# Kernel tuning notes

Hardware: AMD Instinct MI355X
Metric: run time of the kernel (lower is better)

Reference implementation:

```python
import jax, jax.numpy as jnp
import numpy as np
from jax import lax

B, C, H, W = 2, 64, 64, 64


def _conv1x1(x, w, b):
    # w: [Cout, Cin], x: [B, Cin, H, W]
    return jnp.einsum('oi,bihw->bohw', w, x) + b[None, :, None, None]


def _conv3x3(x, w, b):
    # w: [Cout, Cin, 3, 3]
    y = lax.conv_general_dilated(x, w, (1, 1), 'SAME',
                                 dimension_numbers=('NCHW', 'OIHW', 'NCHW'))
    return y + b[None, :, None, None]


def _bn(x, s, b, m, v, eps=1e-5):
    # eval-mode batchnorm with running stats
    inv = s / jnp.sqrt(v + eps)
    return x * inv[None, :, None, None] + (b - m * inv)[None, :, None, None]


def _prelu(x, a):
    return jnp.where(x > 0, x, a * x)


def _forward(x, g,
             pam_q_w, pam_q_b, pam_k_w, pam_k_b, pam_v_w, pam_v_b,
             pam_qg_w, pam_qg_b, pam_kg_w, pam_kg_b, gamma_p,
             se_fc1_w, se_fc2_w, gamma_c,
             pconv1_w, pconv1_b, pbn1_s, pbn1_b, pbn1_m, pbn1_v, pprelu1,
             pconv2_w, pconv2_b, pbn2_s, pbn2_b, pbn2_m, pbn2_v, pprelu2,
             cconv1_w, cconv1_b, cbn1_s, cbn1_b, cbn1_m, cbn1_v, cprelu1,
             cconv2_w, cconv2_b, cbn2_s, cbn2_b, cbn2_m, cbn2_v, cprelu2,
             fconv_w, fconv_b, fbn_s, fbn_b, fbn_m, fbn_v, fprelu):
    b, c, h, w = x.shape
    n = h * w
    sm = jax.nn.softmax
    # ---- G_PAM: position attention with guided double softmax ----
    q = _conv1x1(x, pam_q_w, pam_q_b).reshape(b, c, n)
    k = _conv1x1(x, pam_k_w, pam_k_b).reshape(b, c, n)
    v = _conv1x1(x, pam_v_w, pam_v_b).reshape(b, c, n)
    qg = _conv1x1(g, pam_qg_w, pam_qg_b).reshape(b, -1, n)
    kg = _conv1x1(g, pam_kg_w, pam_kg_b).reshape(b, -1, n)
    att = sm(jnp.einsum('bcn,bcm->bnm', q, k), axis=-1)        # [B,N,N]
    att_g = sm(jnp.einsum('bcn,bcm->bnm', qg, kg), axis=-1)    # [B,N,N]
    gatt = sm(jnp.einsum('bnk,bkm->bnm', att, att_g), axis=-1) # [B,N,N]
    pam_o = jnp.einsum('bcm,bnm->bcn', v, gatt).reshape(b, c, h, w)
    pam = gamma_p * pam_o + x
    # ---- pconv head ----
    t = _prelu(_bn(_conv3x3(pam, pconv1_w, pconv1_b), pbn1_s, pbn1_b, pbn1_m, pbn1_v), pprelu1)
    pam2 = _prelu(_bn(_conv1x1(t, pconv2_w, pconv2_b), pbn2_s, pbn2_b, pbn2_m, pbn2_v), pprelu2)
    # ---- G_CAM: channel attention with SE-gated guide ----
    xq = pam2.reshape(b, c, n)
    att_c = sm(jnp.einsum('bcn,bdn->bcd', xq, xq), axis=-1)    # [B,C,C]
    gy = g.mean((2, 3))  # SE: [B,C]
    gy = jax.nn.sigmoid(jnp.einsum('oc,bc->bo', se_fc2_w,
                                   jax.nn.relu(jnp.einsum('rc,bc->br', se_fc1_w, gy))))
    gq = (g * gy[:, :, None, None]).reshape(b, c, n)
    att_cg = sm(jnp.einsum('bcn,bdn->bcd', gq, gq), axis=-1)   # [B,C,C]
    ge = jnp.einsum('bck,bkd->bcd', att_c, att_cg)
    ge = jnp.max(ge, axis=-1, keepdims=True) - ge
    gatt_c = sm(ge, axis=-1)
    cam_o = jnp.einsum('bcd,bdn->bcn', gatt_c, xq).reshape(b, c, h, w)
    cam = gamma_c * cam_o + pam2
    # ---- cconv + fconv heads ----
    t = _prelu(_bn(_conv3x3(cam, cconv1_w, cconv1_b), cbn1_s, cbn1_b, cbn1_m, cbn1_v), cprelu1)
    cam2 = _prelu(_bn(_conv1x1(t, cconv2_w, cconv2_b), cbn2_s, cbn2_b, cbn2_m, cbn2_v), cprelu2)
    final = _prelu(_bn(_conv1x1(cam2, fconv_w, fconv_b), fbn_s, fbn_b, fbn_m, fbn_v), fprelu)
    return final


def setup_inputs() -> dict:
    key = jax.random.key(0)
    keys = iter(jax.random.split(key, 64))
    nk = lambda: next(keys)
    f32 = jnp.float32
    nrm = lambda shape, s=0.1: s * jax.random.normal(nk(), shape, f32)
    d = {}
    d['x'] = jax.random.normal(nk(), (B, C, H, W), f32)
    d['g'] = jax.random.normal(nk(), (B, C, H, W), f32)
    for p in ['pam_q', 'pam_k', 'pam_v', 'pam_qg', 'pam_kg']:
        d[p + '_w'] = nrm((C, C))
        d[p + '_b'] = nrm((C,))
    d['gamma_p'] = jnp.asarray(0.5, f32)
    d['se_fc1_w'] = nrm((C // 2, C))
    d['se_fc2_w'] = nrm((C, C // 2))
    d['gamma_c'] = jnp.asarray(0.5, f32)
    for pre in ['p', 'c']:
        d[pre + 'conv1_w'] = nrm((C, C, 3, 3), 0.05)
        d[pre + 'conv1_b'] = nrm((C,))
        d[pre + 'bn1_s'] = 1.0 + nrm((C,))
        d[pre + 'bn1_b'] = nrm((C,))
        d[pre + 'bn1_m'] = nrm((C,))
        d[pre + 'bn1_v'] = 1.0 + 0.1 * jax.random.uniform(nk(), (C,), f32)
        d[pre + 'prelu1'] = jnp.asarray(0.25, f32)
        d[pre + 'conv2_w'] = nrm((C, C))
        d[pre + 'conv2_b'] = nrm((C,))
        d[pre + 'bn2_s'] = 1.0 + nrm((C,))
        d[pre + 'bn2_b'] = nrm((C,))
        d[pre + 'bn2_m'] = nrm((C,))
        d[pre + 'bn2_v'] = 1.0 + 0.1 * jax.random.uniform(nk(), (C,), f32)
        d[pre + 'prelu2'] = jnp.asarray(0.25, f32)
    d['fconv_w'] = nrm((C, C))
    d['fconv_b'] = nrm((C,))
    d['fbn_s'] = 1.0 + nrm((C,))
    d['fbn_b'] = nrm((C,))
    d['fbn_m'] = nrm((C,))
    d['fbn_v'] = 1.0 + 0.1 * jax.random.uniform(nk(), (C,), f32)
    d['fprelu'] = jnp.asarray(0.25, f32)
    return d


def reference(x, g,
              pam_q_w, pam_q_b, pam_k_w, pam_k_b, pam_v_w, pam_v_b,
              pam_qg_w, pam_qg_b, pam_kg_w, pam_kg_b, gamma_p,
              se_fc1_w, se_fc2_w, gamma_c,
              pconv1_w, pconv1_b, pbn1_s, pbn1_b, pbn1_m, pbn1_v, pprelu1,
              pconv2_w, pconv2_b, pbn2_s, pbn2_b, pbn2_m, pbn2_v, pprelu2,
              cconv1_w, cconv1_b, cbn1_s, cbn1_b, cbn1_m, cbn1_v, cprelu1,
              cconv2_w, cconv2_b, cbn2_s, cbn2_b, cbn2_m, cbn2_v, cprelu2,
              fconv_w, fconv_b, fbn_s, fbn_b, fbn_m, fbn_v, fprelu):
    return _forward(x, g,
                    pam_q_w, pam_q_b, pam_k_w, pam_k_b, pam_v_w, pam_v_b,
                    pam_qg_w, pam_qg_b, pam_kg_w, pam_kg_b, gamma_p,
                    se_fc1_w, se_fc2_w, gamma_c,
                    pconv1_w, pconv1_b, pbn1_s, pbn1_b, pbn1_m, pbn1_v, pprelu1,
                    pconv2_w, pconv2_b, pbn2_s, pbn2_b, pbn2_m, pbn2_v, pprelu2,
                    cconv1_w, cconv1_b, cbn1_s, cbn1_b, cbn1_m, cbn1_v, cprelu1,
                    cconv2_w, cconv2_b, cbn2_s, cbn2_b, cbn2_m, cbn2_v, cprelu2,
                    fconv_w, fconv_b, fbn_s, fbn_b, fbn_m, fbn_v, fprelu)
```

## Files before the change

### kernel.cpp

```cpp
#include <hip/hip_runtime.h>
#include <hip/hip_fp8.h>


typedef float f32x4 __attribute__((ext_vector_type(4)));
typedef __bf16 bf16x8 __attribute__((ext_vector_type(8)));
typedef int int4v __attribute__((ext_vector_type(4)));
typedef int int8v __attribute__((ext_vector_type(8)));
typedef unsigned short ushort8 __attribute__((ext_vector_type(8)));
typedef unsigned char uchar8 __attribute__((ext_vector_type(8)));

#define DI __device__ __forceinline__

DI float bf2f(unsigned short u) { union { unsigned int i; float f; } x; x.i = ((unsigned int)u) << 16; return x.f; }
DI unsigned short f2bf(float f) { union { float f; unsigned int i; } x; x.f = f; unsigned int r = x.i + 0x7fff + ((x.i >> 16) & 1); return (unsigned short)(r >> 16); }
DI unsigned char f2fp8(float f) { __hip_fp8_e4m3 h(f); return (unsigned char)h.__x; }
DI float sane(float x) { return (x > -1e8f) ? ((x < 1e8f) ? x : 1e8f) : -1e8f; }

DI void async16(const unsigned short* g, unsigned short* l) {
    __builtin_amdgcn_global_load_lds(
        (const __attribute__((address_space(1))) void*)g,
        (__attribute__((address_space(3))) void*)l, 16, 0, 0);
}
DI void async16b(const unsigned char* g, unsigned char* l) {
    __builtin_amdgcn_global_load_lds(
        (const __attribute__((address_space(1))) void*)g,
        (__attribute__((address_space(3))) void*)l, 16, 0, 0);
}

__global__ __launch_bounds__(256) void diag_fill(float* __restrict__ out, int n, float val)
{
    int i = blockIdx.x * 256 + threadIdx.x;
    if (i < n) out[i] = val;
}

__global__ __launch_bounds__(256) void gemm_score(
    const unsigned short* __restrict__ A,
    const unsigned short* __restrict__ B,
    unsigned short* __restrict__ C, int N, long abStride, long cStride)
{
    A += (long)blockIdx.z * abStride;
    B += (long)blockIdx.z * abStride;
    C += (long)blockIdx.z * cStride;
    const int tid  = threadIdx.x;
    const int bm   = blockIdx.y, bn = blockIdx.x;
    const int lane = tid & 63, wid = tid >> 6;
    const int wm   = (wid >> 1) * 64, wn = (wid & 1) * 64;
    const int l16  = lane & 15, quad = lane >> 4;

    f32x4 acc[4][4] = {};
    bf16x8 af[2][4], bfr[2][4];
    #pragma unroll
    for (int w = 0; w < 2; w++) {
        #pragma unroll
        for (int i = 0; i < 4; i++)
            af[w][i]  = *(const bf16x8*)&A[(long)(bm * 128 + wm + i * 16 + l16) * 64 + w * 32 + quad * 8];
        #pragma unroll
        for (int j = 0; j < 4; j++)
            bfr[w][j] = *(const bf16x8*)&B[(long)(bn * 128 + wn + j * 16 + l16) * 64 + w * 32 + quad * 8];
    }
    #pragma unroll
    for (int w = 0; w < 2; w++)
        #pragma unroll
        for (int i = 0; i < 4; i++)
            #pragma unroll
            for (int j = 0; j < 4; j++)
                acc[i][j] = __builtin_amdgcn_mfma_f32_16x16x32_bf16(af[w][i], bfr[w][j], acc[i][j], 0, 0, 0);

    #pragma unroll
    for (int i = 0; i < 4; i++) {
        int rb = bm * 128 + wm + i * 16 + quad * 4;
        #pragma unroll
        for (int j = 0; j < 4; j++) {
            int col = bn * 128 + wn + j * 16 + l16;
            #pragma unroll
            for (int r = 0; r < 4; r++)
                C[(long)(rb + r) * N + col] = f2bf(acc[i][j][r]);
        }
    }
}

__global__ __launch_bounds__(256, 3) void gemm_nt(
    const unsigned short* __restrict__ A,
    const unsigned short* __restrict__ B,
    float* __restrict__ C,
    int M, int N, int K, long sA, long sB, long sC)
{
    A += (long)blockIdx.z * sA;
    B += (long)blockIdx.z * sB;
    C += (long)blockIdx.z * sC;
    __shared__ __align__(16) unsigned short As[128 * 32];
    __shared__ __align__(16) unsigned short Bs[128 * 32];
    const int tid  = threadIdx.x;
    const int bn   = blockIdx.x, slice = blockIdx.y;
    const int lane = tid & 63, wid = tid >> 6;
    const int wm   = (wid >> 1) * 64, wn = (wid & 1) * 64;
    const int l16  = lane & 15, quad = lane >> 4;

    f32x4 acc[4][4] = {};

    const int Kc   = K / (int)gridDim.y;
    const int kbeg = slice * Kc;
    const int nIter = Kc / 32;

    const int row0 = tid >> 2,        cp0 = tid & 3;
    const int row1 = (tid + 256) >> 2, cp1 = (tid + 256) & 3;
    int ar0 = row0; if (ar0 > M - 1) ar0 = M - 1;
    int ar1 = row1; if (ar1 > M - 1) ar1 = M - 1;
    const unsigned short* pa0 = &A[(long)ar0 * K + kbeg + ((cp0 ^ (row0 & 3)) * 8)];
    const unsigned short* pa1 = &A[(long)ar1 * K + kbeg + ((cp1 ^ (row1 & 3)) * 8)];
    const unsigned short* pb0 = &B[(long)(bn * 128 + row0) * K + kbeg + ((cp0 ^ (row0 & 3)) * 8)];
    const unsigned short* pb1 = &B[(long)(bn * 128 + row1) * K + kbeg + ((cp1 ^ (row1 & 3)) * 8)];
    unsigned short* la0 = &As[row0 * 32 + cp0 * 8];
    unsigned short* la1 = &As[row1 * 32 + cp1 * 8];
    unsigned short* lb0 = &Bs[row0 * 32 + cp0 * 8];
    unsigned short* lb1 = &Bs[row1 * 32 + cp1 * 8];

    const int sw = (quad ^ (l16 & 3)) * 8;

    for (int it = 0; it < nIter; it++) {
        __syncthreads();
        async16(pa0, la0);
        async16(pa1, la1);
        async16(pb0, lb0);
        async16(pb1, lb1);
        pa0 += 32; pa1 += 32; pb0 += 32; pb1 += 32;
        __syncthreads();
        bf16x8 af[4], bfr[4];
        #pragma unroll
        for (int i = 0; i < 4; i++) af[i]  = *(const bf16x8*)&As[(wm + i * 16 + l16) * 32 + sw];
        #pragma unroll
        for (int j = 0; j < 4; j++) bfr[j] = *(const bf16x8*)&Bs[(wn + j * 16 + l16) * 32 + sw];
        #pragma unroll
        for (int i = 0; i < 4; i++)
            #pragma unroll
            for (int j = 0; j < 4; j++)
                acc[i][j] = __builtin_amdgcn_mfma_f32_16x16x32_bf16(af[i], bfr[j], acc[i][j], 0, 0, 0);
    }

    #pragma unroll
    for (int i = 0; i < 4; i++) {
        int rb = wm + i * 16 + quad * 4;
        #pragma unroll
        for (int j = 0; j < 4; j++) {
            int col = bn * 128 + wn + j * 16 + l16;
            #pragma unroll
            for (int r = 0; r < 4; r++) {
                int row = rb + r;
                if (row < M)
                    C[(long)slice * M * N + (long)row * N + col] = acc[i][j][r];
            }
        }
    }
}

__global__ __launch_bounds__(256, 2) void gemm_p8(
    const unsigned char* __restrict__ A,
    const unsigned char* __restrict__ B,
    unsigned short* __restrict__ C, int N, int K,
    long sA, long sB, long sC)
{
    A += (long)blockIdx.z * sA;
    B += (long)blockIdx.z * sB;
    C += (long)blockIdx.z * sC;
    __shared__ __align__(16) unsigned char As[128 * 256];
    __shared__ __align__(16) unsigned char Bs[128 * 256];
    const int tid  = threadIdx.x;
    const int bm   = blockIdx.y, bn = blockIdx.x;
    const int lane = tid & 63, wid = tid >> 6;
    const int wm   = (wid >> 1) * 64, wn = (wid & 1) * 64;
    const int l16  = lane & 15, quad = lane >> 4;

    f32x4 acc[4][4] = {};

    const int srow = tid >> 4;
    const int sp   = tid & 15;
    const int cp   = sp ^ (srow & 15);
    const unsigned char* pa = &A[(long)(bm * 128 + srow) * K + cp * 16];
    const unsigned char* pb = &B[(long)(bn * 128 + srow) * K + cp * 16];
    unsigned char* la = &As[srow * 256 + sp * 16];
    unsigned char* lb = &Bs[srow * 256 + sp * 16];
    const long gstep = 16L * K;

    const int nIter = K / 256;
    for (int it = 0; it < nIter; it++) {
        __syncthreads();
        #pragma unroll
        for (int m = 0; m < 8; m++) {
            async16b(pa + m * gstep, la + m * 4096);
            async16b(pb + m * gstep, lb + m * 4096);
        }
        pa += 256; pb += 256;
        __syncthreads();
        #pragma unroll
        for (int h = 0; h < 2; h++) {
            const int c0 = h * 8 + 2 * quad;
            const int s0 = (c0 ^ (l16 & 15)) * 16;
            const int s1 = ((c0 + 1) ^ (l16 & 15)) * 16;
            int8v bfr[4];
            #pragma unroll
            for (int j = 0; j < 4; j++) {
                const unsigned char* base = &Bs[(wn + j * 16 + l16) * 256];
                int4v v0 = *(const int4v*)(base + s0);
                int4v v1 = *(const int4v*)(base + s1);
                bfr[j][0] = v0[0]; bfr[j][1] = v0[1]; bfr[j][2] = v0[2]; bfr[j][3] = v0[3];
                bfr[j][4] = v1[0]; bfr[j][5] = v1[1]; bfr[j][6] = v1[2]; bfr[j][7] = v1[3];
            }
            #pragma unroll
            for (int i = 0; i < 4; i++) {
                const unsigned char* base = &As[(wm + i * 16 + l16) * 256];
                int4v v0 = *(const int4v*)(base + s0);
                int4v v1 = *(const int4v*)(base + s1);
                int8v af;
                af[0] = v0[0]; af[1] = v0[1]; af[2] = v0[2]; af[3] = v0[3];
                af[4] = v1[0]; af[5] = v1[1]; af[6] = v1[2]; af[7] = v1[3];
                #pragma unroll
                for (int j = 0; j < 4; j++)
                    acc[i][j] = __builtin_amdgcn_mfma_scale_f32_16x16x128_f8f6f4(
                        af, bfr[j], acc[i][j],
                        0, 0, 0, 0x7f7f7f7f, 0, 0x7f7f7f7f);
            }
        }
    }

    const float ds = 1.f / 65536.f;
    #pragma unroll
    for (int i = 0; i < 4; i++) {
        int rb = bm * 128 + wm + i * 16 + quad * 4;
        #pragma unroll
        for (int j = 0; j < 4; j++) {
            int col = bn * 128 + wn + j * 16 + l16;
            #pragma unroll
            for (int r = 0; r < 4; r++)
                C[(long)(rb + r) * N + col] = f2bf(acc[i][j][r] * ds);
        }
    }
}

__global__ __launch_bounds__(256) void row_softmax(unsigned short* __restrict__ buf, long bStride)
{
    unsigned short* p = buf + (long)blockIdx.y * bStride + (long)blockIdx.x * 4096;
    const int tid = threadIdx.x, lane = tid & 63, wid = tid >> 6;
    float v[16]; float mx = -1e30f;
    #pragma unroll
    for (int t = 0; t < 16; t++) {
        float x = sane(bf2f(p[t * 256 + tid]));
        v[t] = x; mx = fmaxf(mx, x);
    }
    #pragma unroll
    for (int o = 32; o; o >>= 1) mx = fmaxf(mx, __shfl_xor(mx, o, 64));
    __shared__ float rmax[4], rsum[4];
    if (!lane) rmax[wid] = mx;
    __syncthreads();
    mx = fmaxf(fmaxf(rmax[0], rmax[1]), fmaxf(rmax[2], rmax[3]));
    float s = 0.f;
    #pragma unroll
    for (int t = 0; t < 16; t++) { v[t] = __expf(v[t] - mx); s += v[t]; }
    #pragma unroll
    for (int o = 32; o; o >>= 1) s += __shfl_xor(s, o, 64);
    if (!lane) rsum[wid] = s;
    __syncthreads();
    s = rsum[0] + rsum[1] + rsum[2] + rsum[3];
    float inv = 1.f / s;
    #pragma unroll
    for (int t = 0; t < 16; t++) p[t * 256 + tid] = f2bf(v[t] * inv);
}

__global__ __launch_bounds__(256) void row_softmax_f8(
    const unsigned short* __restrict__ in, unsigned char* __restrict__ out,
    long inStride, long outStride)
{
    const unsigned short* p = in + (long)blockIdx.y * inStride + (long)blockIdx.x * 4096;
    unsigned char* q = out + (long)blockIdx.y * outStride + (long)blockIdx.x * 4096;
    const int tid = threadIdx.x, lane = tid & 63, wid = tid >> 6;
    float v[16]; float mx = -1e30f;
    #pragma unroll
    for (int t = 0; t < 16; t++) {
        float x = sane(bf2f(p[t * 256 + tid]));
        v[t] = x; mx = fmaxf(mx, x);
    }
    #pragma unroll
    for (int o = 32; o; o >>= 1) mx = fmaxf(mx, __shfl_xor(mx, o, 64));
    __shared__ float rmax[4], rsum[4];
    if (!lane) rmax[wid] = mx;
    __syncthreads();
    mx = fmaxf(fmaxf(rmax[0], rmax[1]), fmaxf(rmax[2], rmax[3]));
    float s = 0.f;
    #pragma unroll
    for (int t = 0; t < 16; t++) { v[t] = __expf(v[t] - mx); s += v[t]; }
    #pragma unroll
    for (int o = 32; o; o >>= 1) s += __shfl_xor(s, o, 64);
    if (!lane) rsum[wid] = s;
    __syncthreads();
    s = rsum[0] + rsum[1] + rsum[2] + rsum[3];
    float inv = 256.f / s;
    #pragma unroll
    for (int t = 0; t < 16; t++) q[t * 256 + tid] = f2fp8(v[t] * inv);
}

__global__ __launch_bounds__(256) void colsm_partial(
    const unsigned short* __restrict__ buf,
    float* __restrict__ pmx, float* __restrict__ psum,
    long bufStride, long pStride)
{
    buf  += (long)blockIdx.z * bufStride;
    pmx  += (long)blockIdx.z * pStride;
    psum += (long)blockIdx.z * pStride;
    const int tid = threadIdx.x;
    const int colgrp = tid & 63, rg = tid >> 6;
    const int cbase = blockIdx.x * 512 + colgrp * 8;
    const int r0 = blockIdx.y * 128 + rg * 32;
    const unsigned short* p = buf + (long)r0 * 4096 + cbase;
    float mx[8], s[8];
    #pragma unroll
    for (int j = 0; j < 8; j++) { mx[j] = -1e30f; s[j] = 0.f; }
    for (int r = 0; r < 32; r++) {
        ushort8 v = *(const ushort8*)(p + (long)r * 4096);
        #pragma unroll
        for (int j = 0; j < 8; j++) {
            float x = sane(bf2f(v[j]));
            float nm = fmaxf(mx[j], x);
            s[j] = s[j] * __expf(mx[j] - nm) + __expf(x - nm);
            mx[j] = nm;
        }
    }
    __shared__ float smx[4][512], ssm[4][512];
    #pragma unroll
    for (int j = 0; j < 8; j++) { smx[rg][colgrp * 8 + j] = mx[j]; ssm[rg][colgrp * 8 + j] = s[j]; }
    __syncthreads();
    for (int c = tid; c < 512; c += 256) {
        float M = fmaxf(fmaxf(smx[0][c], smx[1][c]), fmaxf(smx[2][c], smx[3][c]));
        float S = 0.f;
        #pragma unroll
        for (int i = 0; i < 4; i++) S += ssm[i][c] * __expf(smx[i][c] - M);
        int col = blockIdx.x * 512 + c;
        pmx[blockIdx.y * 4096 + col] = M;
        psum[blockIdx.y * 4096 + col] = S;
    }
}

__global__ __launch_bounds__(256) void colsm_norm_f8(
    const unsigned short* __restrict__ in, unsigned char* __restrict__ out,
    const float* __restrict__ pmx, const float* __restrict__ psum,
    long inStride, long outStride, long pStride)
{
    in   += (long)blockIdx.z * inStride;
    out  += (long)blockIdx.z * outStride;
    pmx  += (long)blockIdx.z * pStride;
    psum += (long)blockIdx.z * pStride;
    const int tid = threadIdx.x;
    const int colgrp = tid & 63, rg = tid >> 6;
    const int cbase = blockIdx.x * 512 + colgrp * 8;
    const int r0 = blockIdx.y * 128 + rg * 32;
    const unsigned short* p = in + (long)r0 * 4096 + cbase;
    unsigned char* q = out + (long)r0 * 4096 + cbase;
    float M[8], inv[8];
    #pragma unroll
    for (int j = 0; j < 8; j++) M[j] = -1e30f;
    for (int ch = 0; ch < 32; ch++) {
        #pragma unroll
        for (int j = 0; j < 8; j++) M[j] = fmaxf(M[j], pmx[ch * 4096 + cbase + j]);
    }
    float S[8];
    #pragma unroll
    for (int j = 0; j < 8; j++) S[j] = 0.f;
    for (int ch = 0; ch < 32; ch++) {
        #pragma unroll
        for (int j = 0; j < 8; j++)
            S[j] += psum[ch * 4096 + cbase + j] * __expf(pmx[ch * 4096 + cbase + j] - M[j]);
    }
    #pragma unroll
    for (int j = 0; j < 8; j++) inv[j] = 256.f / S[j];
    for (int r = 0; r < 32; r++) {
        ushort8 v = *(const ushort8*)(p + (long)r * 4096);
        uchar8 o;
        #pragma unroll
        for (int j = 0; j < 8; j++) o[j] = f2fp8(__expf(sane(bf2f(v[j])) - M[j]) * inv[j]);
        *(uchar8*)(q + (long)r * 4096) = o;
    }
}

__global__ __launch_bounds__(256) void proj_x3(
    const float* __restrict__ X,
    const float* __restrict__ Wq, const float* __restrict__ bq,
    const float* __restrict__ Wk, const float* __restrict__ bk,
    const float* __restrict__ Wv, const float* __restrict__ bv,
    unsigned short* __restrict__ qT, unsigned short* __restrict__ kT,
    unsigned short* __restrict__ vC)
{
    const int b = blockIdx.y, nt = blockIdx.x, tid = threadIdx.x;
    __shared__ float Xs[64][64];
    __shared__ float Wqs[64][65];
    __shared__ float Wks[64][65];
    __shared__ float Wvs[64][64];
    __shared__ float Bq[64], Bk[64], Bv[64];
    for (int f = tid; f < 4096; f += 256) {
        int i = f >> 6, n = f & 63;
        Xs[i][n] = X[((long)b * 64 + i) * 4096 + nt * 64 + n];
        Wqs[f & 63][f >> 6] = Wq[f];
        Wks[f & 63][f >> 6] = Wk[f];
        Wvs[f >> 6][f & 63] = Wv[f];
    }
    if (tid < 64) { Bq[tid] = bq[tid]; Bk[tid] = bk[tid]; Bv[tid] = bv[tid]; }
    __syncthreads();
    const int c = tid & 63, g = tid >> 6;
    {
        float acc[16];
        #pragma unroll
        for (int j = 0; j < 16; j++) acc[j] = Bq[c];
        for (int i = 0; i < 64; i++) {
            float wv = Wqs[i][c];
            #pragma unroll
            for (int j = 0; j < 16; j++) acc[j] += wv * Xs[i][g + 4 * j];
        }
        unsigned short* ob = qT + ((long)b * 4096 + nt * 64) * 64;
        #pragma unroll
        for (int j = 0; j < 16; j++) ob[(g + 4 * j) * 64 + c] = f2bf(acc[j]);
    }
    {
        float acc[16];
        #pragma unroll
        for (int j = 0; j < 16; j++) acc[j] = Bk[c];
        for (int i = 0; i < 64; i++) {
            float wv = Wks[i][c];
            #pragma unroll
            for (int j = 0; j < 16; j++) acc[j] += wv * Xs[i][g + 4 * j];
        }
        unsigned short* ob = kT + ((long)b * 4096 + nt * 64) * 64;
        #pragma unroll
        for (int j = 0; j < 16; j++) ob[(g + 4 * j) * 64 + c] = f2bf(acc[j]);
    }
    {
        const int n = tid & 63, gg = tid >> 6;
        float acc[16];
        #pragma unroll
        for (int j = 0; j < 16; j++) acc[j] = Bv[gg + 4 * j];
        for (int i = 0; i < 64; i++) {
            float xv = Xs[i][n];
            #pragma unroll
            for (int j = 0; j < 16; j++) acc[j] += Wvs[gg + 4 * j][i] * xv;
        }
        unsigned short* ob = vC + ((long)b * 64) * 4096 + nt * 64;
        #pragma unroll
        for (int j = 0; j < 16; j++) ob[(long)(gg + 4 * j) * 4096 + n] = f2bf(acc[j]);
    }
}

__global__ __launch_bounds__(256) void proj_g2(
    const float* __restrict__ G,
    const float* __restrict__ Wq, const float* __restrict__ bq,
    const float* __restrict__ Wk, const float* __restrict__ bk,
    unsigned short* __restrict__ qgT, unsigned short* __restrict__ kgT)
{
    const int b = blockIdx.y, nt = blockIdx.x, tid = threadIdx.x;
    __shared__ float Xs[64][64];
    __shared__ float Wqs[64][65];
    __shared__ float Wks[64][65];
    __shared__ float Bq[64], Bk[64];
    for (int f = tid; f < 4096; f += 256) {
        int i = f >> 6, n = f & 63;
        Xs[i][n] = G[((long)b * 64 + i) * 4096 + nt * 64 + n];
        Wqs[f & 63][f >> 6] = Wq[f];
        Wks[f & 63][f >> 6] = Wk[f];
    }
    if (tid < 64) { Bq[tid] = bq[tid]; Bk[tid] = bk[tid]; }
    __syncthreads();
    const int c = tid & 63, g = tid >> 6;
    {
        float acc[16];
        #pragma unroll
        for (int j = 0; j < 16; j++) acc[j] = Bq[c];
        for (int i = 0; i < 64; i++) {
            float wv = Wqs[i][c];
            #pragma unroll
            for (int j = 0; j < 16; j++) acc[j] += wv * Xs[i][g + 4 * j];
        }
        unsigned short* ob = qgT + ((long)b * 4096 + nt * 64) * 64;
        #pragma unroll
        for (int j = 0; j < 16; j++) ob[(g + 4 * j) * 64 + c] = f2bf(acc[j]);
    }
    {
        float acc[16];
        #pragma unroll
        for (int j = 0; j < 16; j++) acc[j] = Bk[c];
        for (int i = 0; i < 64; i++) {
            float wv = Wks[i][c];
            #pragma unroll
            for (int j = 0; j < 16; j++) acc[j] += wv * Xs[i][g + 4 * j];
        }
        unsigned short* ob = kgT + ((long)b * 4096 + nt * 64) * 64;
        #pragma unroll
        for (int j = 0; j < 16; j++) ob[(g + 4 * j) * 64 + c] = f2bf(acc[j]);
    }
}

__global__ __launch_bounds__(256) void combine_pam(
    const float* __restrict__ part, const float* __restrict__ x,
    const float* __restrict__ gammaPtr, float* __restrict__ pam, int nsplit,
    long sPart, long sX)
{
    part += (long)blockIdx.y * sPart;
    x    += (long)blockIdx.y * sX;
    pam  += (long)blockIdx.y * sX;
    int i = blockIdx.x * 256 + threadIdx.x;
    float s = 0.f;
    for (int k = 0; k < nsplit; k++) s += part[(long)k * 262144 + i];
    pam[i] = gammaPtr[0] * s + x[i];
}

__global__ __launch_bounds__(256) void conv3x3_bn(
    const float* __restrict__ X, const float* __restrict__ W9,
    const float* __restrict__ bias,
    const float* __restrict__ bns, const float* __restrict__ bnb,
    const float* __restrict__ bnm, const float* __restrict__ bnv,
    const float* __restrict__ prelu, float* __restrict__ out)
{
    const int b = blockIdx.y, h = blockIdx.x, co0 = blockIdx.z * 16, tid = threadIdx.x;
    __shared__ float Ls[3][64][66];
    __shared__ float ep0[64], ep1[64], ep2[64];
    __shared__ float alpha;
    for (int f = tid; f < 3 * 64 * 64; f += 256) {
        int ky = f >> 12, rem = f & 4095, ci = rem >> 6, w = rem & 63;
        int hh = h + ky - 1;
        Ls[ky][ci][w + 1] = (hh >= 0 && hh < 64) ? X[(((long)b * 64 + ci) * 64 + hh) * 64 + w] : 0.f;
    }
    for (int f = tid; f < 192; f += 256) {
        int ky = f >> 6, ci = f & 63;
        Ls[ky][ci][0] = 0.f; Ls[ky][ci][65] = 0.f;
    }
    if (tid < 64) {
        float inv = bns[tid] * rsqrtf(fmaxf(bnv[tid], 0.f) + 1e-5f);
        ep0[tid] = inv; ep1[tid] = bnb[tid] - bnm[tid] * inv; ep2[tid] = bias[tid];
    }
    if (tid == 0) alpha = prelu[0];
    __syncthreads();
    const int w = tid & 63, g = tid >> 6;
    float acc[4];
    #pragma unroll
    for (int j = 0; j < 4; j++) acc[j] = ep2[co0 + g * 4 + j];
    for (int ci = 0; ci < 64; ci++) {
        float v0 = Ls[0][ci][w], v1 = Ls[0][ci][w + 1], v2 = Ls[0][ci][w + 2];
        float v3 = Ls[1][ci][w], v4 = Ls[1][ci][w + 1], v5 = Ls[1][ci][w + 2];
        float v6 = Ls[2][ci][w], v7 = Ls[2][ci][w + 1], v8 = Ls[2][ci][w + 2];
        #pragma unroll
        for (int j = 0; j < 4; j++) {
            const float* wp = &W9[((co0 + g * 4 + j) * 64 + ci) * 9];
            acc[j] += wp[0] * v0 + wp[1] * v1 + wp[2] * v2
                    + wp[3] * v3 + wp[4] * v4 + wp[5] * v5
                    + wp[6] * v6 + wp[7] * v7 + wp[8] * v8;
        }
    }
    #pragma unroll
    for (int j = 0; j < 4; j++) {
        int co = co0 + g * 4 + j;
        float y = acc[j] * ep0[co] + ep1[co];
        y = y > 0.f ? y : alpha * y;
        out[(((long)b * 64 + co) * 64 + h) * 64 + w] = y;
    }
}

__global__ __launch_bounds__(256) void conv1x1_bn(
    const float* __restrict__ X, const float* __restrict__ W,
    const float* __restrict__ bias,
    const float* __restrict__ bns, const float* __restrict__ bnb,
    const float* __restrict__ bnm, const float* __restrict__ bnv,
    const float* __restrict__ prelu, float* __restrict__ out)
{
    const int b = blockIdx.y, nt = blockIdx.x, co0 = blockIdx.z * 16, tid = threadIdx.x;
    __shared__ float Xs[64][64];
    __shared__ float Ws[16][64];
    __shared__ float ep0[16], ep1[16], ep2[16];
    __shared__ float alpha;
    for (int f = tid; f < 4096; f += 256) {
        int i = f >> 6, n = f & 63;
        Xs[i][n] = X[((long)b * 64 + i) * 4096 + nt * 64 + n];
    }
    for (int f = tid; f < 1024; f += 256)
        Ws[f >> 6][f & 63] = W[(co0 + (f >> 6)) * 64 + (f & 63)];
    if (tid < 16) {
        int c = co0 + tid;
        float inv = bns[c] * rsqrtf(fmaxf(bnv[c], 0.f) + 1e-5f);
        ep0[tid] = inv; ep1[tid] = bnb[c] - bnm[c] * inv; ep2[tid] = bias[c];
    }
    if (tid == 0) alpha = prelu[0];
    __syncthreads();
    const int n = tid & 63, g = tid >> 6;
    float acc[4];
    #pragma unroll
    for (int j = 0; j < 4; j++) acc[j] = ep2[g * 4 + j];
    for (int i = 0; i < 64; i++) {
        float xv = Xs[i][n];
        #pragma unroll
        for (int j = 0; j < 4; j++) acc[j] += Ws[g * 4 + j][i] * xv;
    }
    #pragma unroll
    for (int j = 0; j < 4; j++) {
        int lc = g * 4 + j;
        float y = acc[j] * ep0[lc] + ep1[lc];
        y = y > 0.f ? y : alpha * y;
        out[((long)b * 64 + co0 + lc) * 4096 + nt * 64 + n] = y;
    }
}

__global__ __launch_bounds__(256) void conv1x1x2(
    const float* __restrict__ X,
    const float* __restrict__ W1, const float* __restrict__ b1,
    const float* __restrict__ s1, const float* __restrict__ bb1,
    const float* __restrict__ m1, const float* __restrict__ v1,
    const float* __restrict__ p1,
    const float* __restrict__ W2, const float* __restrict__ b2,
    const float* __restrict__ s2, const float* __restrict__ bb2,
    const float* __restrict__ m2, const float* __restrict__ v2,
    const float* __restrict__ p2,
    float* __restrict__ out)
{
    const int b = blockIdx.y, nt = blockIdx.x, tid = threadIdx.x;
    __shared__ float Xs[64][33];
    __shared__ float Y1[64][33];
    __shared__ float W1s[64][64], W2s[64][64];
    __shared__ float e0a[64], e1a[64], e2a[64], e0b[64], e1b[64], e2b[64];
    __shared__ float al1, al2;
    for (int f = tid; f < 2048; f += 256) {
        int i = f >> 5, n = f & 31;
        Xs[i][n] = X[((long)b * 64 + i) * 4096 + nt * 32 + n];
    }
    for (int f = tid; f < 4096; f += 256) {
        W1s[f >> 6][f & 63] = W1[f];
        W2s[f >> 6][f & 63] = W2[f];
    }
    if (tid < 64) {
        float inv = s1[tid] * rsqrtf(fmaxf(v1[tid], 0.f) + 1e-5f);
        e0a[tid] = inv; e1a[tid] = bb1[tid] - m1[tid] * inv; e2a[tid] = b1[tid];
        inv = s2[tid] * rsqrtf(fmaxf(v2[tid], 0.f) + 1e-5f);
        e0b[tid] = inv; e1b[tid] = bb2[tid] - m2[tid] * inv; e2b[tid] = b2[tid];
    }
    if (tid == 0) { al1 = p1[0]; al2 = p2[0]; }
    __syncthreads();
    const int n = tid & 31, g = tid >> 5;
    float acc[8];
    #pragma unroll
    for (int j = 0; j < 8; j++) acc[j] = e2a[g * 8 + j];
    for (int i = 0; i < 64; i++) {
        float xv = Xs[i][n];
        #pragma unroll
        for (int j = 0; j < 8; j++) acc[j] += W1s[g * 8 + j][i] * xv;
    }
    #pragma unroll
    for (int j = 0; j < 8; j++) {
        int c = g * 8 + j;
        float y = acc[j] * e0a[c] + e1a[c];
        Y1[c][n] = y > 0.f ? y : al1 * y;
    }
    __syncthreads();
    #pragma unroll
    for (int j = 0; j < 8; j++) acc[j] = e2b[g * 8 + j];
    for (int i = 0; i < 64; i++) {
        float xv = Y1[i][n];
        #pragma unroll
        for (int j = 0; j < 8; j++) acc[j] += W2s[g * 8 + j][i] * xv;
    }
    #pragma unroll
    for (int j = 0; j < 8; j++) {
        int c = g * 8 + j;
        float y = acc[j] * e0b[c] + e1b[c];
        y = y > 0.f ? y : al2 * y;
        out[((long)b * 64 + c) * 4096 + nt * 32 + n] = y;
    }
}

__global__ __launch_bounds__(256) void gram_partial(
    const float* __restrict__ X, float* __restrict__ out, float* __restrict__ gy)
{
    const int ch = blockIdx.x, b = blockIdx.y, tid = threadIdx.x;
    __shared__ float Xs[64][33];
    for (int f = tid; f < 2048; f += 256) {
        int ci = f >> 5, kk = f & 31;
        Xs[ci][kk] = X[((long)b * 64 + ci) * 4096 + ch * 32 + kk];
    }
    __syncthreads();
    const int d = tid & 63, g = tid >> 6;
    float acc[16] = {};
    for (int kk = 0; kk < 32; kk++) {
        float xd = Xs[d][kk];
        #pragma unroll
        for (int j = 0; j < 16; j++) acc[j] += Xs[g + 4 * j][kk] * xd;
    }
    #pragma unroll
    for (int j = 0; j < 16; j++)
        atomicAdd(&out[((long)b * 64 + (g + 4 * j)) * 64 + d], acc[j]);
    if (gy && tid < 64) {
        float s = 0.f;
        for (int kk = 0; kk < 32; kk++) s += Xs[tid][kk];
        atomicAdd(&gy[b * 64 + tid], s);
    }
}

__global__ __launch_bounds__(64) void cam_small(
    const float* __restrict__ gramx, const float* __restrict__ gramg,
    const float* __restrict__ gy_in, const float* __restrict__ fc1,
    const float* __restrict__ fc2, float* __restrict__ gattc)
{
    const int b = blockIdx.x, tid = threadIdx.x;
    __shared__ float Ac[64][65], Acg[64][65];
    __shared__ float gyv[64], r1[32], gys[64];
    gyv[tid] = gy_in[b * 64 + tid] * (1.f / 4096.f);
    __syncthreads();
    if (tid < 32) {
        float s = 0.f;
        for (int c = 0; c < 64; c++) s += fc1[tid * 64 + c] * gyv[c];
        r1[tid] = fmaxf(s, 0.f);
    }
    __syncthreads();
    {
        float s = 0.f;
        for (int r = 0; r < 32; r++) s += fc2[tid * 32 + r] * r1[r];
        gys[tid] = 1.f / (1.f + __expf(-sane(s)));
    }
    __syncthreads();
    {
        const float* r = gramx + ((long)b * 64 + tid) * 64;
        float mx = -1e30f;
        for (int d = 0; d < 64; d++) mx = fmaxf(mx, sane(r[d]));
        float s = 0.f;
        for (int d = 0; d < 64; d++) s += __expf(sane(r[d]) - mx);
        float inv = 1.f / s;
        for (int d = 0; d < 64; d++) Ac[tid][d] = __expf(sane(r[d]) - mx) * inv;
    }
    {
        const float* r = gramg + ((long)b * 64 + tid) * 64;
        float gc = gys[tid];
        float mx = -1e30f;
        for (int d = 0; d < 64; d++) mx = fmaxf(mx, sane(gc * gys[d] * r[d]));
        float s = 0.f;
        for (int d = 0; d < 64; d++) s += __expf(sane(gc * gys[d] * r[d]) - mx);
        float inv = 1.f / s;
        for (int d = 0; d < 64; d++) Acg[tid][d] = __expf(sane(gc * gys[d] * r[d]) - mx) * inv;
    }
    __syncthreads();
    float ge[64];
    float mx1 = -1e30f, mn = 1e30f;
    for (int d = 0; d < 64; d++) {
        float s = 0.f;
        for (int k = 0; k < 64; k++) s += Ac[tid][k] * Acg[k][d];
        ge[d] = s;
        mx1 = fmaxf(mx1, s); mn = fminf(mn, s);
    }
    float M2 = mx1 - mn;
    float s = 0.f;
    for (int d = 0; d < 64; d++) s += __expf((mx1 - ge[d]) - M2);
    float inv = 1.f / s;
    for (int d = 0; d < 64; d++)
        gattc[((long)b * 64 + tid) * 64 + d] = __expf((mx1 - ge[d]) - M2) * inv;
}

__global__ __launch_bounds__(256) void cam_apply(
    const float* __restrict__ pam2, const float* __restrict__ gattc,
    const float* __restrict__ gammaPtr, float* __restrict__ cam)
{
    const int b = blockIdx.y, nt = blockIdx.x, co0 = blockIdx.z * 16, tid = threadIdx.x;
    __shared__ float Xs[64][64];
    __shared__ float Gt[16][64];
    for (int f = tid; f < 4096; f += 256) {
        int d = f >> 6, n = f & 63;
        Xs[d][n] = pam2[((long)b * 64 + d) * 4096 + nt * 64 + n];
    }
    for (int f = tid; f < 1024; f += 256)
        Gt[f >> 6][f & 63] = gattc[((long)b * 64 + co0 + (f >> 6)) * 64 + (f & 63)];
    __syncthreads();
    const float gamma = gammaPtr[0];
    const int n = tid & 63, g = tid >> 6;
    float acc[4] = {};
    for (int d = 0; d < 64; d++) {
        float xv = Xs[d][n];
        #pragma unroll
        for (int j = 0; j < 4; j++) acc[j] += Gt[g * 4 + j][d] * xv;
    }
    #pragma unroll
    for (int j = 0; j < 4; j++) {
        int c = co0 + g * 4 + j;
        cam[((long)b * 64 + c) * 4096 + nt * 64 + n] = gamma * acc[j] + Xs[c][n];
    }
}

extern "C" void kernel_launch(void* const* d_in, const int* in_sizes, int n_in,
                              void* d_out, int out_size, void* d_ws, size_t ws_size,
                              hipStream_t stream)
{
    static const int exp_sizes[51] = {
        524288, 524288,
        4096, 64, 4096, 64, 4096, 64, 4096, 64, 4096, 64,
        1, 2048, 2048, 1,
        36864, 64, 64, 64, 64, 64, 1,
        4096, 64, 64, 64, 64, 64, 1,
        36864, 64, 64, 64, 64, 64, 1,
        4096, 64, 64, 64, 64, 64, 1,
        4096, 64, 64, 64, 64, 64, 1
    };
    bool map_ok = (n_in == 51) && (out_size == 524288);
    if (map_ok) for (int i = 0; i < 51; i++) if (in_sizes[i] != exp_sizes[i]) { map_ok = false; break; }

    const int diag_grid = (out_size + 255) / 256;
    if (!map_ok) {
        diag_fill<<<diag_grid, 256, 0, stream>>>((float*)d_out, out_size, 400.0f);
        return;
    }
    const size_t NEED_FULL = 121000000;
    if (ws_size < NEED_FULL) {
        float code = (ws_size >= 88000000) ? 100.0f : (ws_size >= 55000000 ? 200.0f : 300.0f);
        diag_fill<<<diag_grid, 256, 0, stream>>>((float*)d_out, out_size, code);
        return;
    }
    const bool big = (ws_size >= 248000000);
    const int nb = big ? 2 : 1;
    const long NN = 4096L * 4096;

    auto IN = [&](int i) { return (const float*)d_in[i]; };
    const float* X = IN(0);
    const float* G = IN(1);

    char* wp_ = (char*)d_ws;
    auto alloc = [&](size_t bytes) -> void* {
        void* p = (void*)wp_;
        wp_ += (bytes + 255) & ~(size_t)255;
        return p;
    };
    unsigned short* qT   = (unsigned short*)alloc(2L * 4096 * 64 * 2);
    unsigned short* kT   = (unsigned short*)alloc(2L * 4096 * 64 * 2);
    unsigned short* qgT  = (unsigned short*)alloc(2L * 4096 * 64 * 2);
    unsigned short* kgT  = (unsigned short*)alloc(2L * 4096 * 64 * 2);
    unsigned short* vC   = (unsigned short*)alloc(2L * 64 * 4096 * 2);
    float* part  = (float*)alloc((8L * nb) * 64 * 4096 * 4);
    float* pam   = (float*)alloc(2L * 64 * 4096 * 4);
    float* tbuf  = (float*)alloc(2L * 64 * 4096 * 4);
    float* pam2  = (float*)alloc(2L * 64 * 4096 * 4);
    float* cam   = (float*)alloc(2L * 64 * 4096 * 4);
    float* gramx = (float*)alloc(2L * 64 * 64 * 4);
    float* gramg = (float*)alloc(2L * 64 * 64 * 4);
    float* gy    = (float*)alloc(2L * 64 * 4);
    float* gattc = (float*)alloc(2L * 64 * 64 * 4);
    float* pmx   = (float*)alloc((32L * nb) * 4096 * 4);
    float* psum  = (float*)alloc((32L * nb) * 4096 * 4);
    unsigned short* pbuf   = (unsigned short*)alloc(NN * 2 * nb);
    unsigned short* attS   = (unsigned short*)alloc(NN * 2 * nb);
    unsigned char*  attF8  = (unsigned char*)alloc(NN * nb);
    unsigned char*  attgF8 = (unsigned char*)alloc(NN * nb);

    proj_x3<<<dim3(64, 2), 256, 0, stream>>>(X, IN(2), IN(3), IN(4), IN(5), IN(6), IN(7), qT, kT, vC);
    proj_g2<<<dim3(64, 2), 256, 0, stream>>>(G, IN(8), IN(9), IN(10), IN(11), qgT, kgT);

    const long abStr = 4096L * 64;
    const long pStr  = big ? NN : 0;
    const long pmStr = big ? 32L * 4096 : 0;
    for (int b = 0; b < 2; b += nb) {
        const unsigned short* qTb  = qT  + (long)b * abStr;
        const unsigned short* kTb  = kT  + (long)b * abStr;
        const unsigned short* qgTb = qgT + (long)b * abStr;
        const unsigned short* kgTb = kgT + (long)b * abStr;
        gemm_score<<<dim3(32, 32, nb), 256, 0, stream>>>(qTb,  kTb,  pbuf, 4096, abStr, pStr);
        gemm_score<<<dim3(32, 32, nb), 256, 0, stream>>>(kgTb, qgTb, attS, 4096, abStr, pStr);
        row_softmax_f8<<<dim3(4096, nb), 256, 0, stream>>>(pbuf, attF8, pStr, pStr);
        colsm_partial<<<dim3(8, 32, nb), 256, 0, stream>>>(attS, pmx, psum, pStr, pmStr);
        colsm_norm_f8<<<dim3(8, 32, nb), 256, 0, stream>>>(attS, attgF8, pmx, psum, pStr, pStr, pmStr);
        gemm_p8<<<dim3(32, 32, nb), 256, 0, stream>>>(attF8, attgF8, pbuf, 4096, 4096, pStr, pStr, pStr);
        row_softmax<<<dim3(4096, nb), 256, 0, stream>>>(pbuf, pStr);
        gemm_nt<<<dim3(32, 8, nb), 256, 0, stream>>>(vC + (long)b * abStr, pbuf, part,
                                                     64, 4096, 4096,
                                                     abStr, pStr, big ? 8L * 262144 : 0);
        combine_pam<<<dim3(1024, nb), 256, 0, stream>>>(part, X + (long)b * 262144, IN(12),
                                                        pam + (long)b * 262144, 8,
                                                        big ? 8L * 262144 : 0,
                                                        big ? 262144L : 0);
    }

    conv3x3_bn<<<dim3(64, 2, 4), 256, 0, stream>>>(pam, IN(16), IN(17), IN(18), IN(19), IN(20), IN(21), IN(22), tbuf);
    conv1x1_bn<<<dim3(64, 2, 4), 256, 0, stream>>>(tbuf, IN(23), IN(24), IN(25), IN(26), IN(27), IN(28), IN(29), pam2);

    diag_fill<<<65, 256, 0, stream>>>(gramx, 16384 + 128, 0.0f);
    gram_partial<<<dim3(128, 2), 256, 0, stream>>>(pam2, gramx, nullptr);
    gram_partial<<<dim3(128, 2), 256, 0, stream>>>(G,    gramg, gy);
    cam_small<<<2, 64, 0, stream>>>(gramx, gramg, gy, IN(13), IN(14), gattc);
    cam_apply<<<dim3(64, 2, 4), 256, 0, stream>>>(pam2, gattc, IN(15), cam);

    conv3x3_bn<<<dim3(64, 2, 4), 256, 0, stream>>>(cam, IN(30), IN(31), IN(32), IN(33), IN(34), IN(35), IN(36), pam);
    conv1x1x2<<<dim3(128, 2), 256, 0, stream>>>(pam,
        IN(37), IN(38), IN(39), IN(40), IN(41), IN(42), IN(43),
        IN(44), IN(45), IN(46), IN(47), IN(48), IN(49), IN(50),
        (float*)d_out);
}
```

Before: 657.7 us.

## Compute PAM value GEMM in fp8 with fp8 softmax output and V

Stores the V projection and the final attention softmax in fp8 and replaces the bf16 V×attention GEMM with a new fp8 scaled-MFMA kernel using wider tiles. The combine step applies a descale factor. This halves memory traffic for the attention matrix read and softmax write, but adds fp8 quantization error on V and the attention weights.

```diff
diff --git a/kernel.cpp b/kernel.cpp
--- a/kernel.cpp
+++ b/kernel.cpp
@@ -75,80 +75,6 @@
             #pragma unroll
             for (int r = 0; r < 4; r++)
                 C[(long)(rb + r) * N + col] = f2bf(acc[i][j][r]);
-        }
-    }
-}
-
-__global__ __launch_bounds__(256, 3) void gemm_nt(
-    const unsigned short* __restrict__ A,
-    const unsigned short* __restrict__ B,
-    float* __restrict__ C,
-    int M, int N, int K, long sA, long sB, long sC)
-{
-    A += (long)blockIdx.z * sA;
-    B += (long)blockIdx.z * sB;
-    C += (long)blockIdx.z * sC;
-    __shared__ __align__(16) unsigned short As[128 * 32];
-    __shared__ __align__(16) unsigned short Bs[128 * 32];
-    const int tid  = threadIdx.x;
-    const int bn   = blockIdx.x, slice = blockIdx.y;
-    const int lane = tid & 63, wid = tid >> 6;
-    const int wm   = (wid >> 1) * 64, wn = (wid & 1) * 64;
-    const int l16  = lane & 15, quad = lane >> 4;
-
-    f32x4 acc[4][4] = {};
-
-    const int Kc   = K / (int)gridDim.y;
-    const int kbeg = slice * Kc;
-    const int nIter = Kc / 32;
-
-    const int row0 = tid >> 2,        cp0 = tid & 3;
-    const int row1 = (tid + 256) >> 2, cp1 = (tid + 256) & 3;
-    int ar0 = row0; if (ar0 > M - 1) ar0 = M - 1;
-    int ar1 = row1; if (ar1 > M - 1) ar1 = M - 1;
-    const unsigned short* pa0 = &A[(long)ar0 * K + kbeg + ((cp0 ^ (row0 & 3)) * 8)];
-    const unsigned short* pa1 = &A[(long)ar1 * K + kbeg + ((cp1 ^ (row1 & 3)) * 8)];
-    const unsigned short* pb0 = &B[(long)(bn * 128 + row0) * K + kbeg + ((cp0 ^ (row0 & 3)) * 8)];
-    const unsigned short* pb1 = &B[(long)(bn * 128 + row1) * K + kbeg + ((cp1 ^ (row1 & 3)) * 8)];
-    unsigned short* la0 = &As[row0 * 32 + cp0 * 8];
-    unsigned short* la1 = &As[row1 * 32 + cp1 * 8];
-    unsigned short* lb0 = &Bs[row0 * 32 + cp0 * 8];
-    unsigned short* lb1 = &Bs[row1 * 32 + cp1 * 8];
-
-    const int sw = (quad ^ (l16 & 3)) * 8;
-
-    for (int it = 0; it < nIter; it++) {
-        __syncthreads();
-        async16(pa0, la0);
-        async16(pa1, la1);
-        async16(pb0, lb0);
-        async16(pb1, lb1);
-        pa0 += 32; pa1 += 32; pb0 += 32; pb1 += 32;
-        __syncthreads();
-        bf16x8 af[4], bfr[4];
-        #pragma unroll
-        for (int i = 0; i < 4; i++) af[i]  = *(const bf16x8*)&As[(wm + i * 16 + l16) * 32 + sw];
-        #pragma unroll
-        for (int j = 0; j < 4; j++) bfr[j] = *(const bf16x8*)&Bs[(wn + j * 16 + l16) * 32 + sw];
-        #pragma unroll
-        for (int i = 0; i < 4; i++)
-            #pragma unroll
-            for (int j = 0; j < 4; j++)
-                acc[i][j] = __builtin_amdgcn_mfma_f32_16x16x32_bf16(af[i], bfr[j], acc[i][j], 0, 0, 0);
-    }
-
-    #pragma unroll
-    for (int i = 0; i < 4; i++) {
-        int rb = wm + i * 16 + quad * 4;
-        #pragma unroll
-        for (int j = 0; j < 4; j++) {
-            int col = bn * 128 + wn + j * 16 + l16;
-            #pragma unroll
-            for (int r = 0; r < 4; r++) {
-                int row = rb + r;
-                if (row < M)
-                    C[(long)slice * M * N + (long)row * N + col] = acc[i][j][r];
-            }
         }
     }
 }
@@ -236,33 +162,87 @@
     }
 }
 
-__global__ __launch_bounds__(256) void row_softmax(unsigned short* __restrict__ buf, long bStride)
-{
-    unsigned short* p = buf + (long)blockIdx.y * bStride + (long)blockIdx.x * 4096;
-    const int tid = threadIdx.x, lane = tid & 63, wid = tid >> 6;
-    float v[16]; float mx = -1e30f;
-    #pragma unroll
-    for (int t = 0; t < 16; t++) {
-        float x = sane(bf2f(p[t * 256 + tid]));
-        v[t] = x; mx = fmaxf(mx, x);
-    }
-    #pragma unroll
-    for (int o = 32; o; o >>= 1) mx = fmaxf(mx, __shfl_xor(mx, o, 64));
-    __shared__ float rmax[4], rsum[4];
-    if (!lane) rmax[wid] = mx;
-    __syncthreads();
-    mx = fmaxf(fmaxf(rmax[0], rmax[1]), fmaxf(rmax[2], rmax[3]));
-    float s = 0.f;
-    #pragma unroll
-    for (int t = 0; t < 16; t++) { v[t] = __expf(v[t] - mx); s += v[t]; }
-    #pragma unroll
-    for (int o = 32; o; o >>= 1) s += __shfl_xor(s, o, 64);
-    if (!lane) rsum[wid] = s;
-    __syncthreads();
-    s = rsum[0] + rsum[1] + rsum[2] + rsum[3];
-    float inv = 1.f / s;
-    #pragma unroll
-    for (int t = 0; t < 16; t++) p[t * 256 + tid] = f2bf(v[t] * inv);
+__global__ __launch_bounds__(256, 2) void gemm_p8_pam(
+    const unsigned char* __restrict__ A,
+    const unsigned char* __restrict__ B,
+    float* __restrict__ C,
+    int N, int K, long sA, long sB, long sC)
+{
+    A += (long)blockIdx.z * sA;
+    B += (long)blockIdx.z * sB;
+    C += (long)blockIdx.z * sC;
+    __shared__ __align__(16) unsigned char As[64 * 128];
+    __shared__ __align__(16) unsigned char Bs[256 * 128];
+    const int tid  = threadIdx.x;
+    const int bn   = blockIdx.x, slice = blockIdx.y;
+    const int lane = tid & 63, wid = tid >> 6;
+    const int wn   = wid * 64;
+    const int l16  = lane & 15, quad = lane >> 4;
+
+    f32x4 acc[4][4] = {};
+
+    const int Kc   = K / (int)gridDim.y;
+    const int kbeg = slice * Kc;
+
+    const int arow = tid >> 3, asp = tid & 7, acp = asp ^ (arow & 7);
+    const int brow = tid >> 3, bsp = tid & 7, bcp = bsp ^ (brow & 7);
+    const unsigned char* pa = &A[(long)(arow) * K + kbeg + acp * 16];
+    const unsigned char* pb = &B[(long)(bn * 256 + brow) * K + kbeg + bcp * 16];
+    unsigned char* la = &As[arow * 128 + asp * 16];
+    unsigned char* lb = &Bs[brow * 128 + bsp * 16];
+    const long gstepA = 32L * K;
+    const long gstepB = 32L * K;
+
+    const int s0 = ((2 * quad) ^ (l16 & 7)) * 16;
+    const int s1 = ((2 * quad + 1) ^ (l16 & 7)) * 16;
+
+    const int nIter = Kc / 128;
+    for (int it = 0; it < nIter; it++) {
+        __syncthreads();
+        #pragma unroll
+        for (int m = 0; m < 2; m++)
+            async16b(pa + m * gstepA, la + m * 4096);
+        #pragma unroll
+        for (int m = 0; m < 8; m++)
+            async16b(pb + m * gstepB, lb + m * 4096);
+        pa += 128; pb += 128;
+        __syncthreads();
+        int8v bfr[4];
+        #pragma unroll
+        for (int j = 0; j < 4; j++) {
+            const unsigned char* base = &Bs[(wn + j * 16 + l16) * 128];
+            int4v v0 = *(const int4v*)(base + s0);
+            int4v v1 = *(const int4v*)(base + s1);
+            bfr[j][0] = v0[0]; bfr[j][1] = v0[1]; bfr[j][2] = v0[2]; bfr[j][3] = v0[3];
+            bfr[j][4] = v1[0]; bfr[j][5] = v1[1]; bfr[j][6] = v1[2]; bfr[j][7] = v1[3];
+        }
+        #pragma unroll
+        for (int i = 0; i < 4; i++) {
+            const unsigned char* base = &As[(i * 16 + l16) * 128];
+            int4v v0 = *(const int4v*)(base + s0);
+            int4v v1 = *(const int4v*)(base + s1);
+            int8v af;
+            af[0] = v0[0]; af[1] = v0[1]; af[2] = v0[2]; af[3] = v0[3];
+            af[4] = v1[0]; af[5] = v1[1]; af[6] = v1[2]; af[7] = v1[3];
+            #pragma unroll
+            for (int j = 0; j < 4; j++)
+                acc[i][j] = __builtin_amdgcn_mfma_scale_f32_16x16x128_f8f6f4(
+                    af, bfr[j], acc[i][j],
+                    0, 0, 0, 0x7f7f7f7f, 0, 0x7f7f7f7f);
+        }
+    }
+
+    #pragma unroll
+    for (int i = 0; i < 4; i++) {
+        int rb = i * 16 + quad * 4;
+        #pragma unroll
+        for (int j = 0; j < 4; j++) {
+            int col = bn * 256 + wn + j * 16 + l16;
+            #pragma unroll
+            for (int r = 0; r < 4; r++)
+                C[(long)slice * 64 * N + (long)(rb + r) * N + col] = acc[i][j][r];
+        }
+    }
 }
 
 __global__ __launch_bounds__(256) void row_softmax_f8(
@@ -385,7 +365,7 @@
     const float* __restrict__ Wk, const float* __restrict__ bk,
     const float* __restrict__ Wv, const float* __restrict__ bv,
     unsigned short* __restrict__ qT, unsigned short* __restrict__ kT,
-    unsigned short* __restrict__ vC)
+    unsigned char* __restrict__ vC8)
 {
     const int b = blockIdx.y, nt = blockIdx.x, tid = threadIdx.x;
     __shared__ float Xs[64][64];
@@ -439,9 +419,9 @@
             #pragma unroll
             for (int j = 0; j < 16; j++) acc[j] += Wvs[gg + 4 * j][i] * xv;
         }
-        unsigned short* ob = vC + ((long)b * 64) * 4096 + nt * 64;
-        #pragma unroll
-        for (int j = 0; j < 16; j++) ob[(long)(gg + 4 * j) * 4096 + n] = f2bf(acc[j]);
+        unsigned char* ob = vC8 + ((long)b * 64) * 4096 + nt * 64;
+        #pragma unroll
+        for (int j = 0; j < 16; j++) ob[(long)(gg + 4 * j) * 4096 + n] = f2fp8(acc[j]);
     }
 }
 
@@ -496,7 +476,7 @@
 __global__ __launch_bounds__(256) void combine_pam(
     const float* __restrict__ part, const float* __restrict__ x,
     const float* __restrict__ gammaPtr, float* __restrict__ pam, int nsplit,
-    long sPart, long sX)
+    long sPart, long sX, float ds)
 {
     part += (long)blockIdx.y * sPart;
     x    += (long)blockIdx.y * sX;
@@ -504,7 +484,7 @@
     int i = blockIdx.x * 256 + threadIdx.x;
     float s = 0.f;
     for (int k = 0; k < nsplit; k++) s += part[(long)k * 262144 + i];
-    pam[i] = gammaPtr[0] * s + x[i];
+    pam[i] = gammaPtr[0] * (s * ds) + x[i];
 }
 
 __global__ __launch_bounds__(256) void conv3x3_bn(
@@ -827,7 +807,7 @@
     unsigned short* kT   = (unsigned short*)alloc(2L * 4096 * 64 * 2);
     unsigned short* qgT  = (unsigned short*)alloc(2L * 4096 * 64 * 2);
     unsigned short* kgT  = (unsigned short*)alloc(2L * 4096 * 64 * 2);
-    unsigned short* vC   = (unsigned short*)alloc(2L * 64 * 4096 * 2);
+    unsigned char*  vC8  = (unsigned char*)alloc(2L * 64 * 4096);
     float* part  = (float*)alloc((8L * nb) * 64 * 4096 * 4);
     float* pam   = (float*)alloc(2L * 64 * 4096 * 4);
     float* tbuf  = (float*)alloc(2L * 64 * 4096 * 4);
@@ -844,7 +824,7 @@
     unsigned char*  attF8  = (unsigned char*)alloc(NN * nb);
     unsigned char*  attgF8 = (unsigned char*)alloc(NN * nb);
 
-    proj_x3<<<dim3(64, 2), 256, 0, stream>>>(X, IN(2), IN(3), IN(4), IN(5), IN(6), IN(7), qT, kT, vC);
+    proj_x3<<<dim3(64, 2), 256, 0, stream>>>(X, IN(2), IN(3), IN(4), IN(5), IN(6), IN(7), qT, kT, vC8);
     proj_g2<<<dim3(64, 2), 256, 0, stream>>>(G, IN(8), IN(9), IN(10), IN(11), qgT, kgT);
 
     const long abStr = 4096L * 64;
@@ -861,14 +841,15 @@
         colsm_partial<<<dim3(8, 32, nb), 256, 0, stream>>>(attS, pmx, psum, pStr, pmStr);
         colsm_norm_f8<<<dim3(8, 32, nb), 256, 0, stream>>>(attS, attgF8, pmx, psum, pStr, pStr, pmStr);
         gemm_p8<<<dim3(32, 32, nb), 256, 0, stream>>>(attF8, attgF8, pbuf, 4096, 4096, pStr, pStr, pStr);
-        row_softmax<<<dim3(4096, nb), 256, 0, stream>>>(pbuf, pStr);
-        gemm_nt<<<dim3(32, 8, nb), 256, 0, stream>>>(vC + (long)b * abStr, pbuf, part,
-                                                     64, 4096, 4096,
-                                                     abStr, pStr, big ? 8L * 262144 : 0);
+        row_softmax_f8<<<dim3(4096, nb), 256, 0, stream>>>(pbuf, attF8, pStr, pStr);
+        gemm_p8_pam<<<dim3(16, 8, nb), 256, 0, stream>>>(vC8 + (long)b * abStr, attF8, part,
+                                                         4096, 4096, abStr, pStr,
+                                                         big ? 8L * 262144 : 0);
         combine_pam<<<dim3(1024, nb), 256, 0, stream>>>(part, X + (long)b * 262144, IN(12),
                                                         pam + (long)b * 262144, 8,
                                                         big ? 8L * 262144 : 0,
-                                                        big ? 262144L : 0);
+                                                        big ? 262144L : 0,
+                                                        1.f / 256.f);
     }
 
     conv3x3_bn<<<dim3(64, 2, 4), 256, 0, stream>>>(pam, IN(16), IN(17), IN(18), IN(19), IN(20), IN(21), IN(22), tbuf);
```

Measured after the change: 653.2 us. No clear change (-0.7%).
